# Kernel optimization log

Hardware: AMD Instinct MI355X
Metric: run time of the kernel (lower is better)

Reference implementation:

```python
import jax, jax.numpy as jnp
import numpy as np

B, T, D, H = 512, 200, 64, 256
C1, C2, C3, R1 = 1024, 256, 10, 1024

def _lin(k, out_d, in_d):
    k1, k2 = jax.random.split(k)
    lim = 1.0 / np.sqrt(in_d)
    w = jax.random.uniform(k1, (out_d, in_d), minval=-lim, maxval=lim, dtype=jnp.float32)
    b = jax.random.uniform(k2, (out_d,), minval=-lim, maxval=lim, dtype=jnp.float32)
    return w, b

def setup_inputs() -> dict:
    key = jax.random.key(0)
    ks = jax.random.split(key, 12)
    lim = 1.0 / np.sqrt(H)
    u = lambda k, sh: jax.random.uniform(k, sh, minval=-lim, maxval=lim, dtype=jnp.float32)
    inp = {"x": jax.random.normal(ks[0], (B, T, D), dtype=jnp.float32)}
    # LSTM layer 0 (input dim D) and layer 1 (input dim H); torch gate order i,f,g,o
    inp["W_ih0"], inp["b_ih0"], inp["b_hh0"] = u(ks[1], (4 * H, D)), u(ks[2], (4 * H,)), u(ks[3], (4 * H,))
    inp["W_ih1"], inp["b_ih1"], inp["b_hh1"] = u(ks[4], (4 * H, H)), u(ks[5], (4 * H,)), u(ks[6], (4 * H,))
    inp["fc1_w"], inp["fc1_b"] = _lin(ks[7], C1, H * T)
    inp["fc2_w"], inp["fc2_b"] = _lin(ks[8], C2, C1)
    inp["fc3_w"], inp["fc3_b"] = _lin(ks[9], C3, C2)
    inp["fc4_w"], inp["fc4_b"] = _lin(ks[10], R1, H * T)
    inp["fc5_w"], inp["fc5_b"] = _lin(ks[11], T, R1)
    return inp

def _lstm_step_zero(x, W_ih, b_ih, b_hh):
    # Single LSTM cell step from h0=c0=0, applied independently to every
    # (batch, timestep) position: gates = x @ W_ih^T + b_ih + b_hh
    gates = jnp.einsum('btd,gd->btg', x, W_ih) + b_ih + b_hh  # [B,T,4H]
    i, f, g, o = jnp.split(gates, 4, axis=-1)  # torch gate order i,f,g,o
    c = jax.nn.sigmoid(i) * jnp.tanh(g)        # c0 = 0 => forget gate irrelevant
    return jax.nn.sigmoid(o) * jnp.tanh(c)

def reference(x, W_ih0, b_ih0, b_hh0, W_ih1, b_ih1, b_hh1,
              fc1_w, fc1_b, fc2_w, fc2_b, fc3_w, fc3_b,
              fc4_w, fc4_b, fc5_w, fc5_b):
    h0 = _lstm_step_zero(x, W_ih0, b_ih0, b_hh0)          # [B,T,H]
    out_total = _lstm_step_zero(h0, W_ih1, b_ih1, b_hh1)  # [B,T,H]
    flat = out_total.reshape(-1, H * T)
    # classification head (dropout = identity in eval)
    c = jax.nn.relu(flat @ fc1_w.T + fc1_b)
    c = jax.nn.relu(c @ fc2_w.T + fc2_b)
    output_class3 = c @ fc3_w.T + fc3_b                   # [B,C3]
    r = jax.nn.relu(flat @ fc4_w.T + fc4_b)
    output_reg3 = (r @ fc5_w.T + fc5_b).reshape(-1, T, 1) # [B,T,1]
    return (out_total, output_class3, output_reg3)
```

## Files before the change

### kernel.cpp

```cpp
#include <hip/hip_runtime.h>
#include <hip/hip_bf16.h>

typedef unsigned short u16;
typedef unsigned int   u32;

typedef __bf16 bf16x8 __attribute__((ext_vector_type(8)));
typedef float  f32x4  __attribute__((ext_vector_type(4)));

__device__ __forceinline__ bf16x8 as_bf16x8(uint4 u) {
    return __builtin_bit_cast(bf16x8, u);
}

__device__ __forceinline__ u16 bf16r(float f) {
    return (u16)((__float_as_uint(f) + 0x8000u) >> 16);
}
__device__ __forceinline__ u32 pack2(float lo, float hi) {
    u32 a = __float_as_uint(lo) + 0x8000u;
    u32 b = __float_as_uint(hi) + 0x8000u;
    return (a >> 16) | (b & 0xFFFF0000u);
}

__device__ __forceinline__ float sigmoidf_(float x) {
    return 1.0f / (1.0f + __expf(-x));
}
__device__ __forceinline__ float tanhf_(float x) {
    float xx = fminf(fmaxf(x, -15.0f), 15.0f);
    float e = __expf(2.0f * xx);
    return (e - 1.0f) / (e + 1.0f);
}

__global__ __launch_bounds__(256) void prep_kernel(
    const float* __restrict__ W_ih0, const float* __restrict__ b_ih0, const float* __restrict__ b_hh0,
    const float* __restrict__ W_ih1, const float* __restrict__ b_ih1, const float* __restrict__ b_hh1,
    u16* __restrict__ Wb0, u16* __restrict__ Wb1, float* __restrict__ bs0, float* __restrict__ bs1)
{
    int idx = blockIdx.x * 256 + threadIdx.x;
    if (idx < 49152) {
        int k = idx & 63, sn = idx >> 6;
        int n = sn & 255, s = sn >> 8;
        int row = (s == 0) ? n : (s == 1 ? 512 + n : 768 + n);
        Wb0[idx] = bf16r(W_ih0[row * 64 + k]);
    } else if (idx < 245760) {
        int j = idx - 49152;
        int k = j & 255, sn = j >> 8;
        int n = sn & 255, s = sn >> 8;
        int row = (s == 0) ? n : (s == 1 ? 512 + n : 768 + n);
        Wb1[j] = bf16r(W_ih1[row * 256 + k]);
    } else if (idx < 247296) {
        int j = idx - 245760;
        int l = j / 768, q = j - l * 768;
        int s = q >> 8, n = q & 255;
        int row = (s == 0) ? n : (s == 1 ? 512 + n : 768 + n);
        if (l == 0) bs0[q] = b_ih0[row] + b_hh0[row];
        else        bs1[q] = b_ih1[row] + b_hh1[row];
    }
}

template<int K, bool IS_L1>
__global__ __launch_bounds__(256) void lstm_kernel(
    const void* __restrict__ xin,
    const u16*  __restrict__ Wb,
    const float* __restrict__ bsum,
    u16*   __restrict__ hout_b,
    float* __restrict__ hout_f)
{
    constexpr int SP = K + 8;
    __shared__ u16 x_s[64 * SP];
    const int t  = threadIdx.x;
    const int m0 = blockIdx.y * 64;
    const int n0 = blockIdx.x * 64;

    if (!IS_L1) {
        const float* xf = (const float*)xin;
        int row = t >> 2, seg = t & 3;
        const float* src = xf + (size_t)(m0 + row) * 64 + seg * 16;
        u32 p0 = pack2(src[0],  src[1]);
        u32 p1 = pack2(src[2],  src[3]);
        u32 p2 = pack2(src[4],  src[5]);
        u32 p3 = pack2(src[6],  src[7]);
        u32 p4 = pack2(src[8],  src[9]);
        u32 p5 = pack2(src[10], src[11]);
        u32 p6 = pack2(src[12], src[13]);
        u32 p7 = pack2(src[14], src[15]);
        u16* dst = x_s + row * SP + seg * 16;
        *(uint4*)(dst)     = make_uint4(p0, p1, p2, p3);
        *(uint4*)(dst + 8) = make_uint4(p4, p5, p6, p7);
    } else {
        const u16* xb = (const u16*)xin;
        #pragma unroll
        for (int p = 0; p < 2; p++) {
            int row = p * 32 + (t >> 3);
            int seg = t & 7;
            const u16* src = xb + (size_t)(m0 + row) * 256 + seg * 32;
            u16* dst = x_s + row * SP + seg * 32;
            #pragma unroll
            for (int i = 0; i < 4; i++)
                *(uint4*)(dst + i * 8) = *(const uint4*)(src + i * 8);
        }
    }
    __syncthreads();

    const int lane = t & 63, w = t >> 6, quad = lane >> 4, l15 = lane & 15;
    const int n = n0 + w * 16 + l15;

    f32x4 acc[3][4] = {};
    #pragma unroll
    for (int kc = 0; kc < K; kc += 32) {
        bf16x8 b[3];
        #pragma unroll
        for (int s = 0; s < 3; s++)
            b[s] = as_bf16x8(*(const uint4*)(Wb + (size_t)(s * 256 + n) * K + kc + quad * 8));
        #pragma unroll
        for (int mt = 0; mt < 4; mt++) {
            bf16x8 a = as_bf16x8(*(const uint4*)(x_s + (mt * 16 + l15) * SP + kc + quad * 8));
            #pragma unroll
            for (int s = 0; s < 3; s++)
                acc[s][mt] = __builtin_amdgcn_mfma_f32_16x16x32_bf16(a, b[s], acc[s][mt], 0, 0, 0);
        }
    }

    const float bi = bsum[n], bg = bsum[256 + n], bo = bsum[512 + n];
    #pragma unroll
    for (int mt = 0; mt < 4; mt++) {
        #pragma unroll
        for (int r = 0; r < 4; r++) {
            int m = m0 + mt * 16 + quad * 4 + r;
            float vi = acc[0][mt][r] + bi;
            float vg = acc[1][mt][r] + bg;
            float vo = acc[2][mt][r] + bo;
            float c  = sigmoidf_(vi) * tanhf_(vg);
            float h  = sigmoidf_(vo) * tanhf_(c);
            size_t off = (size_t)m * 256 + n;
            if (IS_L1) { hout_f[off] = h; hout_b[off] = bf16r(h); }
            else       { hout_b[off] = bf16r(h); }
        }
    }
}

__global__ __launch_bounds__(256) void fc14_kernel(
    const u16* __restrict__ flat,
    const float* __restrict__ w1, const float* __restrict__ w4,
    float* __restrict__ P)
{
    __shared__ u16 A_s[128 * 136];
    const int t  = threadIdx.x;
    const int nb = blockIdx.x, mb = blockIdx.y, z = blockIdx.z;
    const int m0 = mb * 128;
    const float* W = (nb < 8) ? w1 : w4;
    const int wrow0 = (nb & 7) * 128;
    const int lane = t & 63, w = t >> 6, quad = lane >> 4, l15 = lane & 15;
    const long kbase = (long)z * 6400;

    f32x4 acc[8][2] = {};
    const int srow = t >> 1, shalf = t & 1;

    for (int kg = 0; kg < 50; kg++) {
        const long k0 = kbase + (long)kg * 128;
        __syncthreads();
        {
            const u16* src = flat + (size_t)(m0 + srow) * 51200 + k0 + shalf * 64;
            u16* dst = A_s + srow * 136 + shalf * 64;
            #pragma unroll
            for (int i = 0; i < 8; i++)
                *(uint4*)(dst + i * 8) = *(const uint4*)(src + i * 8);
        }
        __syncthreads();
        #pragma unroll
        for (int c = 0; c < 4; c++) {
            const int kc = c * 32;
            bf16x8 b[2];
            #pragma unroll
            for (int nt = 0; nt < 2; nt++) {
                int nrow = wrow0 + w * 32 + nt * 16 + l15;
                const float* wp = W + (size_t)nrow * 51200 + k0 + kc + quad * 8;
                float4 f0 = *(const float4*)(wp);
                float4 f1 = *(const float4*)(wp + 4);
                uint4 u;
                u.x = pack2(f0.x, f0.y); u.y = pack2(f0.z, f0.w);
                u.z = pack2(f1.x, f1.y); u.w = pack2(f1.z, f1.w);
                b[nt] = as_bf16x8(u);
            }
            #pragma unroll
            for (int mt = 0; mt < 8; mt++) {
                bf16x8 a = as_bf16x8(*(const uint4*)(A_s + (mt * 16 + l15) * 136 + kc + quad * 8));
                acc[mt][0] = __builtin_amdgcn_mfma_f32_16x16x32_bf16(a, b[0], acc[mt][0], 0, 0, 0);
                acc[mt][1] = __builtin_amdgcn_mfma_f32_16x16x32_bf16(a, b[1], acc[mt][1], 0, 0, 0);
            }
        }
    }

    float* Pp = P + (size_t)z * (512 * 2048);
    #pragma unroll
    for (int mt = 0; mt < 8; mt++) {
        #pragma unroll
        for (int nt = 0; nt < 2; nt++) {
            int ng = nb * 128 + w * 32 + nt * 16 + l15;
            #pragma unroll
            for (int r = 0; r < 4; r++) {
                int m = m0 + mt * 16 + quad * 4 + r;
                Pp[(size_t)m * 2048 + ng] = acc[mt][nt][r];
            }
        }
    }
}

__global__ __launch_bounds__(256) void reduce_bias_relu(
    const float* __restrict__ P, const float* __restrict__ b1, const float* __restrict__ b4,
    float* __restrict__ c1r)
{
    int idx = blockIdx.x * 256 + threadIdx.x;
    int m = idx >> 9;
    int n = (idx & 511) * 4;
    float4 s = make_float4(0.f, 0.f, 0.f, 0.f);
    #pragma unroll
    for (int z = 0; z < 8; z++) {
        float4 p = *(const float4*)(P + ((size_t)z * 512 + m) * 2048 + n);
        s.x += p.x; s.y += p.y; s.z += p.z; s.w += p.w;
    }
    const float* bp = (n < 1024) ? (b1 + n) : (b4 + (n - 1024));
    float4 b = *(const float4*)bp;
    s.x = fmaxf(s.x + b.x, 0.f);
    s.y = fmaxf(s.y + b.y, 0.f);
    s.z = fmaxf(s.z + b.z, 0.f);
    s.w = fmaxf(s.w + b.w, 0.f);
    *(float4*)(c1r + (size_t)m * 2048 + n) = s;
}

__global__ __launch_bounds__(256) void sgemm_small(
    const float* __restrict__ A, int lda,
    const float* __restrict__ W,
    const float* __restrict__ bias,
    float* __restrict__ out, int ldo,
    int M, int N, int K, int do_relu)
{
    __shared__ float As[16 * 260];
    const int t = threadIdx.x;
    const int m0 = blockIdx.y * 16, n0 = blockIdx.x * 16;
    const int mi = t >> 4, ni = t & 15;
    const int n = n0 + ni;
    const bool act = n < N;
    float acc = 0.f;
    for (int kc = 0; kc < K; kc += 256) {
        __syncthreads();
        {
            int row = t >> 4, cb = (t & 15) * 16;
            const float* src = A + (size_t)(m0 + row) * lda + kc + cb;
            float* dst = As + row * 260 + cb;
            *(float4*)(dst)      = *(const float4*)(src);
            *(float4*)(dst + 4)  = *(const float4*)(src + 4);
            *(float4*)(dst + 8)  = *(const float4*)(src + 8);
            *(float4*)(dst + 12) = *(const float4*)(src + 12);
        }
        __syncthreads();
        if (act) {
            const float* wr = W + (size_t)n * K + kc;
            const float* ar = As + mi * 260;
            #pragma unroll 4
            for (int k = 0; k < 256; k += 4) {
                float4 w4 = *(const float4*)(wr + k);
                float4 a4 = *(const float4*)(ar + k);
                acc += a4.x * w4.x + a4.y * w4.y + a4.z * w4.z + a4.w * w4.w;
            }
        }
    }
    if (act) {
        float v = acc + bias[n];
        if (do_relu) v = fmaxf(v, 0.f);
        out[(size_t)(m0 + mi) * ldo + n] = v;
    }
}

extern "C" void kernel_launch(void* const* d_in, const int* in_sizes, int n_in,
                              void* d_out, int out_size, void* d_ws, size_t ws_size,
                              hipStream_t stream) {
    const float* x      = (const float*)d_in[0];
    const float* W_ih0  = (const float*)d_in[1];
    const float* b_ih0  = (const float*)d_in[2];
    const float* b_hh0  = (const float*)d_in[3];
    const float* W_ih1  = (const float*)d_in[4];
    const float* b_ih1  = (const float*)d_in[5];
    const float* b_hh1  = (const float*)d_in[6];
    const float* fc1_w  = (const float*)d_in[7];
    const float* fc1_b  = (const float*)d_in[8];
    const float* fc2_w  = (const float*)d_in[9];
    const float* fc2_b  = (const float*)d_in[10];
    const float* fc3_w  = (const float*)d_in[11];
    const float* fc3_b  = (const float*)d_in[12];
    const float* fc4_w  = (const float*)d_in[13];
    const float* fc4_b  = (const float*)d_in[14];
    const float* fc5_w  = (const float*)d_in[15];
    const float* fc5_b  = (const float*)d_in[16];
    float* out = (float*)d_out;

    char* ws = (char*)d_ws;
    u16*   Wb0  = (u16*)  (ws + 0);
    u16*   Wb1  = (u16*)  (ws + 98304);
    float* bs0  = (float*)(ws + 491520);
    float* bs1  = (float*)(ws + 494592);
    u16*   h0   = (u16*)  (ws + 524288);
    float* P    = (float*)(ws + 524288);
    u16*   flat = (u16*)  (ws + 52953088);
    float* c1r  = (float*)(ws + 105381888);
    float* c2   = (float*)(ws + 109576192);
    if (ws_size < 110100480) return;

    prep_kernel<<<966, 256, 0, stream>>>(W_ih0, b_ih0, b_hh0, W_ih1, b_ih1, b_hh1,
                                         Wb0, Wb1, bs0, bs1);
    lstm_kernel<64,  false><<<dim3(4, 1600), 256, 0, stream>>>(x,  Wb0, bs0, h0,   nullptr);
    lstm_kernel<256, true ><<<dim3(4, 1600), 256, 0, stream>>>(h0, Wb1, bs1, flat, out);
    fc14_kernel<<<dim3(16, 4, 8), 256, 0, stream>>>(flat, fc1_w, fc4_w, P);
    reduce_bias_relu<<<1024, 256, 0, stream>>>(P, fc1_b, fc4_b, c1r);
    sgemm_small<<<dim3(16, 32), 256, 0, stream>>>(c1r,        2048, fc2_w, fc2_b, c2,             256, 512, 256, 1024, 1);
    sgemm_small<<<dim3(13, 32), 256, 0, stream>>>(c1r + 1024, 2048, fc5_w, fc5_b, out + 26219520, 200, 512, 200, 1024, 0);
    sgemm_small<<<dim3(1,  32), 256, 0, stream>>>(c2,          256, fc3_w, fc3_b, out + 26214400,  10, 512,  10,  256, 0);
}
```

Measured before the change: 1.250 ms.

## Restructure fc1/fc4 GEMM with direct-to-LDS loads, swizzle, smaller N tiles

Reworks the fc1/fc4 split-K GEMM kernel. Each block now covers 64 output columns instead of 128, giving 2x2 waves over a 128x64 tile and twice as many blocks. The activation tile is loaded with global_load_lds straight into an XOR-swizzled, unpadded LDS layout, and the fp32 weight loads for the whole K chunk are issued before the barrier. Weights are converted with the hardware v_cvt_pk_bf16_f32 instruction instead of manual rounding. The aim is better occupancy and latency hiding for this large weight stream, at the cost of reading the activation tile twice as often and relying on the swizzle indexing being correct.

```diff
diff --git a/kernel.cpp b/kernel.cpp
--- a/kernel.cpp
+++ b/kernel.cpp
@@ -18,6 +18,18 @@
     u32 a = __float_as_uint(lo) + 0x8000u;
     u32 b = __float_as_uint(hi) + 0x8000u;
     return (a >> 16) | (b & 0xFFFF0000u);
+}
+
+__device__ __forceinline__ u32 cvtpk(float lo, float hi) {
+    u32 r;
+    asm("v_cvt_pk_bf16_f32 %0, %1, %2" : "=v"(r) : "v"(lo), "v"(hi));
+    return r;
+}
+__device__ __forceinline__ bf16x8 wcvt(float4 a, float4 b) {
+    uint4 u;
+    u.x = cvtpk(a.x, a.y); u.y = cvtpk(a.z, a.w);
+    u.z = cvtpk(b.x, b.y); u.w = cvtpk(b.z, b.w);
+    return as_bf16x8(u);
 }
 
 __device__ __forceinline__ float sigmoidf_(float x) {
@@ -142,62 +154,75 @@
     const float* __restrict__ w1, const float* __restrict__ w4,
     float* __restrict__ P)
 {
-    __shared__ u16 A_s[128 * 136];
+    __shared__ __align__(16) u16 A_s[128 * 128];
     const int t  = threadIdx.x;
-    const int nb = blockIdx.x, mb = blockIdx.y, z = blockIdx.z;
+    const int nb = blockIdx.x;
+    const int mb = blockIdx.y, z = blockIdx.z;
     const int m0 = mb * 128;
-    const float* W = (nb < 8) ? w1 : w4;
-    const int wrow0 = (nb & 7) * 128;
-    const int lane = t & 63, w = t >> 6, quad = lane >> 4, l15 = lane & 15;
-    const long kbase = (long)z * 6400;
-
-    f32x4 acc[8][2] = {};
-    const int srow = t >> 1, shalf = t & 1;
+    const float* W = (nb < 16) ? w1 : w4;
+    const int wrow0 = (nb & 15) * 64;
+
+    const int lane = t & 63, w = t >> 6;
+    const int quad = lane >> 4, l15 = lane & 15;
+    const int wm = w >> 1, wn = w & 1;
+    const int xk = l15 & 7;
+
+    const int rlo = lane >> 4;
+    const int s16 = lane & 15;
+    const int colA = s16 ^ rlo;
+    const int colB = s16 ^ (4 | rlo);
+    const u16* fsrc = flat + (size_t)(m0 + w * 32 + rlo) * 51200 + (size_t)z * 6400;
+
+    const float* wb0 = W + (size_t)(wrow0 + wn * 32 +  0 + l15) * 51200 + (size_t)z * 6400 + quad * 8;
+    const float* wb1 = W + (size_t)(wrow0 + wn * 32 + 16 + l15) * 51200 + (size_t)z * 6400 + quad * 8;
+
+    f32x4 acc[4][2] = {};
 
     for (int kg = 0; kg < 50; kg++) {
-        const long k0 = kbase + (long)kg * 128;
+        const int kk = kg * 128;
         __syncthreads();
-        {
-            const u16* src = flat + (size_t)(m0 + srow) * 51200 + k0 + shalf * 64;
-            u16* dst = A_s + srow * 136 + shalf * 64;
+        #pragma unroll
+        for (int it = 0; it < 8; it++) {
+            const u16* src = fsrc + (size_t)(it * 4) * 51200 + kk
+                           + ((it & 1) ? colB : colA) * 8;
+            u16* dst = A_s + (w * 8 + it) * 512;
+            __builtin_amdgcn_global_load_lds(
+                (const __attribute__((address_space(1))) u16*)src,
+                (__attribute__((address_space(3))) u16*)dst, 16, 0, 0);
+        }
+        float4 wf[4][2][2];
+        #pragma unroll
+        for (int c = 0; c < 4; c++) {
+            wf[c][0][0] = *(const float4*)(wb0 + kk + c * 32);
+            wf[c][0][1] = *(const float4*)(wb0 + kk + c * 32 + 4);
+            wf[c][1][0] = *(const float4*)(wb1 + kk + c * 32);
+            wf[c][1][1] = *(const float4*)(wb1 + kk + c * 32 + 4);
+        }
+        __syncthreads();
+        #pragma unroll
+        for (int c = 0; c < 4; c++) {
+            bf16x8 b0 = wcvt(wf[c][0][0], wf[c][0][1]);
+            bf16x8 b1 = wcvt(wf[c][1][0], wf[c][1][1]);
+            const int soff = ((c * 4 + quad) ^ xk) * 8;
             #pragma unroll
-            for (int i = 0; i < 8; i++)
-                *(uint4*)(dst + i * 8) = *(const uint4*)(src + i * 8);
-        }
-        __syncthreads();
-        #pragma unroll
-        for (int c = 0; c < 4; c++) {
-            const int kc = c * 32;
-            bf16x8 b[2];
-            #pragma unroll
-            for (int nt = 0; nt < 2; nt++) {
-                int nrow = wrow0 + w * 32 + nt * 16 + l15;
-                const float* wp = W + (size_t)nrow * 51200 + k0 + kc + quad * 8;
-                float4 f0 = *(const float4*)(wp);
-                float4 f1 = *(const float4*)(wp + 4);
-                uint4 u;
-                u.x = pack2(f0.x, f0.y); u.y = pack2(f0.z, f0.w);
-                u.z = pack2(f1.x, f1.y); u.w = pack2(f1.z, f1.w);
-                b[nt] = as_bf16x8(u);
-            }
-            #pragma unroll
-            for (int mt = 0; mt < 8; mt++) {
-                bf16x8 a = as_bf16x8(*(const uint4*)(A_s + (mt * 16 + l15) * 136 + kc + quad * 8));
-                acc[mt][0] = __builtin_amdgcn_mfma_f32_16x16x32_bf16(a, b[0], acc[mt][0], 0, 0, 0);
-                acc[mt][1] = __builtin_amdgcn_mfma_f32_16x16x32_bf16(a, b[1], acc[mt][1], 0, 0, 0);
+            for (int mt = 0; mt < 4; mt++) {
+                const int row = wm * 64 + mt * 16 + l15;
+                bf16x8 a = as_bf16x8(*(const uint4*)(A_s + row * 128 + soff));
+                acc[mt][0] = __builtin_amdgcn_mfma_f32_16x16x32_bf16(a, b0, acc[mt][0], 0, 0, 0);
+                acc[mt][1] = __builtin_amdgcn_mfma_f32_16x16x32_bf16(a, b1, acc[mt][1], 0, 0, 0);
             }
         }
     }
 
     float* Pp = P + (size_t)z * (512 * 2048);
     #pragma unroll
-    for (int mt = 0; mt < 8; mt++) {
+    for (int mt = 0; mt < 4; mt++) {
         #pragma unroll
         for (int nt = 0; nt < 2; nt++) {
-            int ng = nb * 128 + w * 32 + nt * 16 + l15;
+            const int ng = nb * 64 + wn * 32 + nt * 16 + l15;
             #pragma unroll
             for (int r = 0; r < 4; r++) {
-                int m = m0 + mt * 16 + quad * 4 + r;
+                const int m = m0 + wm * 64 + mt * 16 + quad * 4 + r;
                 Pp[(size_t)m * 2048 + ng] = acc[mt][nt][r];
             }
         }
@@ -308,7 +333,7 @@
                                          Wb0, Wb1, bs0, bs1);
     lstm_kernel<64,  false><<<dim3(4, 1600), 256, 0, stream>>>(x,  Wb0, bs0, h0,   nullptr);
     lstm_kernel<256, true ><<<dim3(4, 1600), 256, 0, stream>>>(h0, Wb1, bs1, flat, out);
-    fc14_kernel<<<dim3(16, 4, 8), 256, 0, stream>>>(flat, fc1_w, fc4_w, P);
+    fc14_kernel<<<dim3(32, 4, 8), 256, 0, stream>>>(flat, fc1_w, fc4_w, P);
     reduce_bias_relu<<<1024, 256, 0, stream>>>(P, fc1_b, fc4_b, c1r);
     sgemm_small<<<dim3(16, 32), 256, 0, stream>>>(c1r,        2048, fc2_w, fc2_b, c2,             256, 512, 256, 1024, 1);
     sgemm_small<<<dim3(13, 32), 256, 0, stream>>>(c1r + 1024, 2048, fc5_w, fc5_b, out + 26219520, 200, 512, 200, 1024, 0);
```

New measurement: 1.168 ms. 1.07x faster.
